# Optimization experiments

Hardware: AMD Instinct MI355X
Metric: run time of the kernel (lower is better)

Reference implementation:

```python
import jax, jax.numpy as jnp
import numpy as np

B, S, D, H = 4, 1024, 1024, 16
HD = D // H
LN_EPS = 1e-5


def setup_inputs() -> dict:
    key = jax.random.key(0)
    ks = jax.random.split(key, 16)
    def lin(k, fan_in, fan_out):
        bound = 1.0 / np.sqrt(fan_in)
        kw, kb = jax.random.split(k)
        W = jax.random.uniform(kw, (fan_in, fan_out), jnp.float32, -bound, bound)
        b = jax.random.uniform(kb, (fan_out,), jnp.float32, -bound, bound)
        return W, b
    W_attn, b_attn = lin(ks[0], D, 3 * D)   # self-attn fused QKV
    W_Q, b_Q = lin(ks[1], D, D)             # cross-attn Q
    W_KV, b_KV = lin(ks[2], D, 2 * D)       # cross-attn KV
    W1, b1 = lin(ks[3], D, 4 * D)           # FFN up
    W2, b2 = lin(ks[4], 4 * D, D)           # FFN down
    return {
        'en': jax.random.normal(ks[5], (B, S, D), jnp.float32),
        'fr': jax.random.normal(ks[6], (B, S, D), jnp.float32),
        'W_attn': W_attn, 'b_attn': b_attn,
        'W_Q': W_Q, 'b_Q': b_Q, 'W_KV': W_KV, 'b_KV': b_KV,
        'ln_g': jnp.ones((D,), jnp.float32), 'ln_b': jnp.zeros((D,), jnp.float32),
        'W1': W1, 'b1': b1, 'W2': W2, 'b2': b2,
        'l_en': jax.random.randint(ks[7], (B,), 1, S + 1, jnp.int32),
        'l_fr': jax.random.randint(ks[8], (B,), 1, S + 1, jnp.int32),
    }


def _masked_softmax(s):
    # softmax with rows that may be entirely -inf -> all-zero row (torch softmax + nan_to_num)
    m = jnp.max(s, axis=-1, keepdims=True)
    m = jnp.where(jnp.isfinite(m), m, 0.0)
    e = jnp.exp(s - m)  # exp(-inf) = 0
    z = jnp.sum(e, axis=-1, keepdims=True)
    return jnp.where(z > 0, e / jnp.where(z > 0, z, 1.0), 0.0)


def _layer_norm(x, g, b):
    mu = jnp.mean(x, axis=-1, keepdims=True)
    var = jnp.mean((x - mu) ** 2, axis=-1, keepdims=True)
    return (x - mu) * jax.lax.rsqrt(var + LN_EPS) * g + b


def _attend(q, k, v, mask):
    # q,k,v: [B,H,S,hd]; mask: [B,1|H broadcastable,S,S] of {0,1}
    scores = jnp.einsum('bhqd,bhkd->bhqk', q, k) / (D ** 0.5)  # NOTE: scaled by sqrt(D), as in source
    scores = jnp.where(mask == 0, -jnp.inf, scores)
    p = _masked_softmax(scores)
    out = jnp.einsum('bhqk,bhkd->bhqd', p, v)
    return out.transpose(0, 2, 1, 3).reshape(q.shape[0], q.shape[2], D)


def _valid(l):
    return (jnp.arange(S)[None, :] < l[:, None]).astype(jnp.float32)  # [B,S]


def reference(en, fr, W_attn, b_attn, W_Q, b_Q, W_KV, b_KV, ln_g, ln_b, W1, b1, W2, b2, l_en, l_fr):
    # dropout layers are identity in eval/reference mode
    v_en, v_fr = _valid(l_en), _valid(l_fr)

    # --- masked causal self-attention on fr ---
    rc = fr
    qkv = (fr @ W_attn + b_attn).reshape(B, S, 3, H, HD).transpose(2, 0, 3, 1, 4)
    q, k, v = qkv[0], qkv[1], qkv[2]
    pad = (v_fr[:, :, None] * v_fr[:, None, :])[:, None]            # [B,1,S,S]
    causal = jnp.tril(jnp.ones((S, S), jnp.float32))[None, None]    # [1,1,S,S]
    x = _attend(q, k, v, pad * causal)
    fr2 = _layer_norm(x + rc, ln_g, ln_b)

    # --- encoder-decoder cross attention ---
    rc = fr2
    q = (fr2 @ W_Q + b_Q).reshape(B, S, H, HD).transpose(0, 2, 1, 3)
    kv = (en @ W_KV + b_KV).reshape(B, S, 2, H, HD).transpose(2, 0, 3, 1, 4)
    k, v = kv[0], kv[1]
    cross = (v_fr[:, :, None] * v_en[:, None, :])[:, None]          # [B,1,S,S]
    x = _attend(q, k, v, cross)
    fr3 = _layer_norm(x + rc, ln_g, ln_b)

    # --- FFN (Linear->ReLU->Linear) then extra ReLU, residual, LN ---
    rc = fr3
    h = jax.nn.relu(fr3 @ W1 + b1) @ W2 + b2
    h = jax.nn.relu(h)
    fr4 = _layer_norm(h + rc, ln_g, ln_b)
    return fr4
```

## Files before the change

### kernel.cpp

```cpp
#include <hip/hip_runtime.h>
#include <hip/hip_bf16.h>
#include <cstdint>
#include <cstddef>

#define S_LEN  1024
#define DMODEL 1024
#define NHEAD  16
#define HDIM   64
#define BATCH  4
#define MROWS  (BATCH * S_LEN)

typedef __bf16 bf16;
typedef __attribute__((ext_vector_type(8))) __bf16 bf16x8;
typedef __attribute__((ext_vector_type(4))) __bf16 bf16x4;
typedef __attribute__((ext_vector_type(4))) float f32x4;
typedef __attribute__((ext_vector_type(4))) unsigned int u32x4;

__device__ __forceinline__ void async_load16(const void* g, void* l) {
    __builtin_amdgcn_global_load_lds(
        (const __attribute__((address_space(1))) unsigned int*)g,
        (__attribute__((address_space(3))) unsigned int*)l,
        16, 0, 0);
}

__global__ __launch_bounds__(256)
void prep_all(const float* __restrict__ fr, bf16* __restrict__ fr_bf,
              const float* __restrict__ en, bf16* __restrict__ en_bf,
              const float* __restrict__ Wa, bf16* __restrict__ Ta,
              const float* __restrict__ Wkv, bf16* __restrict__ Tkv) {
    __shared__ float t[32][33];
    int id = blockIdx.x;
    if (id < 8192) {
        const int n4 = MROWS * DMODEL / 4;
        int i = id * 256 + threadIdx.x;
        const float* in = fr; bf16* out = fr_bf;
        if (i >= n4) { i -= n4; in = en; out = en_bf; }
        f32x4 v = ((const f32x4*)in)[i];
        bf16x4 o;
#pragma unroll
        for (int e = 0; e < 4; ++e) o[e] = (bf16)v[e];
        ((bf16x4*)out)[i] = o;
        return;
    }
    id -= 8192;
    const float* W; bf16* Wt; int K, N, nx, base;
    if (id < 3072) { W = Wa;  Wt = Ta;  K = 1024; N = 3072; nx = 96; base = 0; }
    else           { W = Wkv; Wt = Tkv; K = 1024; N = 2048; nx = 64; base = 3072; }
    int loc = id - base;
    int n0 = (loc % nx) * 32, k0 = (loc / nx) * 32;
    int tx = threadIdx.x & 31, ty = threadIdx.x >> 5;
#pragma unroll
    for (int j = 0; j < 4; ++j)
        t[ty + j * 8][tx] = W[(size_t)(k0 + ty + j * 8) * N + n0 + tx];
    __syncthreads();
#pragma unroll
    for (int j = 0; j < 4; ++j)
        Wt[(size_t)(n0 + ty + j * 8) * K + k0 + tx] = (bf16)t[tx][ty + j * 8];
}

__device__ __forceinline__ void gemm_acc(const bf16* __restrict__ A,
                                         const bf16* __restrict__ Bt,
                                         int Klen, int lda, int ldb,
                                         bf16* Alds, bf16* Blds,
                                         f32x4 acc[4][4]) {
    const int tid = threadIdx.x;
    const int wave = tid >> 6, lane = tid & 63;
    const int wr = wave >> 1, wc = wave & 1;
    const int lr = lane & 15, lg = lane >> 4, lk = lg * 8;
    const int srow = lane >> 2, scol = (lane & 3) * 8;

    const bf16* Aw = A + (size_t)(wave * 32 + srow) * lda + scol;
    const bf16* Bw = Bt + (size_t)(wave * 32 + srow) * ldb + scol;
    const int ldsw = (wave * 32) * 32;

    async_load16(Aw, Alds + ldsw);
    async_load16(Aw + (size_t)16 * lda, Alds + ldsw + 16 * 32);
    async_load16(Bw, Blds + ldsw);
    async_load16(Bw + (size_t)16 * ldb, Blds + ldsw + 16 * 32);
    __syncthreads();

    const int nt = Klen >> 5;
    for (int t = 0; t < nt; ++t) {
        const int cur = t & 1;
        if (t + 1 < nt) {
            const size_t k0 = (size_t)(t + 1) << 5;
            bf16* Ad = Alds + (cur ^ 1) * (128 * 32) + ldsw;
            bf16* Bd = Blds + (cur ^ 1) * (128 * 32) + ldsw;
            async_load16(Aw + k0, Ad);
            async_load16(Aw + (size_t)16 * lda + k0, Ad + 16 * 32);
            async_load16(Bw + k0, Bd);
            async_load16(Bw + (size_t)16 * ldb + k0, Bd + 16 * 32);
        }
        const bf16* Ab = Alds + cur * (128 * 32);
        const bf16* Bb = Blds + cur * (128 * 32);
        bf16x8 af[4], bfv[4];
#pragma unroll
        for (int i = 0; i < 4; ++i) {
            af[i]  = *(const bf16x8*)&Ab[(wr * 64 + i * 16 + lr) * 32 + lk];
            bfv[i] = *(const bf16x8*)&Bb[(wc * 64 + i * 16 + lr) * 32 + lk];
        }
#pragma unroll
        for (int mi = 0; mi < 4; ++mi)
#pragma unroll
            for (int ni = 0; ni < 4; ++ni)
                acc[mi][ni] = __builtin_amdgcn_mfma_f32_16x16x32_bf16(
                    af[mi], bfv[ni], acc[mi][ni], 0, 0, 0);
        __syncthreads();
    }
}

__device__ __forceinline__ void gemm_acc64(const bf16* __restrict__ A,
                                           const bf16* __restrict__ Bt,
                                           int Klen, int lda, int ldb,
                                           bf16* Alds, bf16* Blds,
                                           f32x4 acc[4][4]) {
    const int tid = threadIdx.x;
    const int wave = tid >> 6, lane = tid & 63;
    const int wr = wave >> 1, wc = wave & 1;
    const int lr = lane & 15, lg = lane >> 4;
    const int srow = lane >> 3;
    const int sch = (lane & 7) ^ srow;

    const bf16* Aw = A + (size_t)(wave * 32 + srow) * lda + sch * 8;
    const bf16* Bw = Bt + (size_t)(wave * 32 + srow) * ldb + sch * 8;

    const int nt = Klen >> 6;
#define STAGE64(buf, k0)                                                       \
    {                                                                          \
        bf16* Ad = Alds + (buf) * (128 * 64) + (wave * 32) * 64;               \
        bf16* Bd = Blds + (buf) * (128 * 64) + (wave * 32) * 64;               \
        _Pragma("unroll")                                                      \
        for (int j = 0; j < 4; ++j) {                                          \
            async_load16(Aw + (size_t)(j * 8) * lda + (k0), Ad + (j * 8) * 64);\
            async_load16(Bw + (size_t)(j * 8) * ldb + (k0), Bd + (j * 8) * 64);\
        }                                                                      \
    }

    STAGE64(0, 0);
    __syncthreads();

    for (int t = 0; t < nt; ++t) {
        const int cur = t & 1;
        if (t + 1 < nt) STAGE64(cur ^ 1, (size_t)(t + 1) << 6);
        const char* Ab = (const char*)(Alds + cur * (128 * 64));
        const char* Bb = (const char*)(Blds + cur * (128 * 64));
#pragma unroll
        for (int ks = 0; ks < 2; ++ks) {
            bf16x8 af[4], bfv[4];
#pragma unroll
            for (int i = 0; i < 4; ++i) {
                int ra = wr * 64 + i * 16 + lr;
                int rb = wc * 64 + i * 16 + lr;
                af[i] = *(const bf16x8*)(Ab + (size_t)ra * 128 +
                          ((ks * 64 + lg * 16) ^ ((ra & 7) << 4)));
                bfv[i] = *(const bf16x8*)(Bb + (size_t)rb * 128 +
                          ((ks * 64 + lg * 16) ^ ((rb & 7) << 4)));
            }
#pragma unroll
            for (int mi = 0; mi < 4; ++mi)
#pragma unroll
                for (int ni = 0; ni < 4; ++ni)
                    acc[mi][ni] = __builtin_amdgcn_mfma_f32_16x16x32_bf16(
                        af[mi], bfv[ni], acc[mi][ni], 0, 0, 0);
        }
        __syncthreads();
    }
#undef STAGE64
}

template<bool RELU>
__device__ __forceinline__ void epi_bf16(bf16* __restrict__ C, const float* __restrict__ bias,
                                         int N, int m0, int n0, f32x4 acc[4][4]) {
    const int tid = threadIdx.x;
    const int wave = tid >> 6, lane = tid & 63;
    const int wr = wave >> 1, wc = wave & 1;
    const int lr = lane & 15, lg = lane >> 4;
#pragma unroll
    for (int ni = 0; ni < 4; ++ni) {
        int n = n0 + wc * 64 + ni * 16 + lr;
        float bn = bias[n];
#pragma unroll
        for (int mi = 0; mi < 4; ++mi)
#pragma unroll
            for (int r = 0; r < 4; ++r) {
                int m = m0 + wr * 64 + mi * 16 + lg * 4 + r;
                float v = acc[mi][ni][r] + bn;
                if (RELU) v = v > 0.f ? v : 0.f;
                C[(size_t)m * N + n] = (bf16)v;
            }
    }
}

__device__ __forceinline__ bool tile_dead(const int* Lm, int m0) {
    if (!Lm) return false;
    int cap = (Lm[m0 >> 10] + 63) & ~63;
    return (m0 & 1023) >= cap;
}

template<bool RELU>
__global__ __launch_bounds__(256, 2)
void gemm_one(const bf16* __restrict__ A, const bf16* __restrict__ Bt,
              const float* __restrict__ bias, bf16* __restrict__ C,
              int N, int K, const int* __restrict__ Lm) {
    __shared__ alignas(16) bf16 Alds[2][128 * 32];
    __shared__ alignas(16) bf16 Blds[2][128 * 32];
    const int nwg = gridDim.x;
    const int flat = blockIdx.x;
    const int swz = (flat & 7) * (nwg >> 3) + (flat >> 3);
    const int m0 = (swz & 31) * 128, n0 = (swz >> 5) * 128;
    if (tile_dead(Lm, m0)) return;
    f32x4 acc[4][4] = {};
    gemm_acc(A + (size_t)m0 * K, Bt + (size_t)n0 * K, K, K, K,
             &Alds[0][0], &Blds[0][0], acc);
    epi_bf16<RELU>(C, bias, N, m0, n0, acc);
}

template<bool RELU>
__global__ __launch_bounds__(256, 2)
void gemm_one64(const bf16* __restrict__ A, const bf16* __restrict__ Bt,
                const float* __restrict__ bias, bf16* __restrict__ C,
                int N, int K, const int* __restrict__ Lm) {
    __shared__ alignas(16) bf16 Alds[2][128 * 64];
    __shared__ alignas(16) bf16 Blds[2][128 * 64];
    const int nwg = gridDim.x;
    const int flat = blockIdx.x;
    const int swz = (flat & 7) * (nwg >> 3) + (flat >> 3);
    const int m0 = (swz & 31) * 128, n0 = (swz >> 5) * 128;
    if (tile_dead(Lm, m0)) return;
    f32x4 acc[4][4] = {};
    gemm_acc64(A + (size_t)m0 * K, Bt + (size_t)n0 * K, K, K, K,
               &Alds[0][0], &Blds[0][0], acc);
    epi_bf16<RELU>(C, bias, N, m0, n0, acc);
}

struct GemmArgs {
    const bf16* A; const bf16* Bt; const float* bias; bf16* C;
    int N; int K; const int* Lm;
};
__global__ __launch_bounds__(256, 2)
void gemm_dual(GemmArgs g0, int nwg0, GemmArgs g1, int nwgG,
               const float* __restrict__ Wq, bf16* __restrict__ Tq,
               const float* __restrict__ W1, bf16* __restrict__ T1,
               const float* __restrict__ W2, bf16* __restrict__ T2) {
    __shared__ alignas(16) bf16 Alds[2][128 * 32];
    __shared__ alignas(16) bf16 Blds[2][128 * 32];
    const int flat = blockIdx.x;
    if (flat >= nwgG) {
        int id = flat - nwgG;
        const float* W; bf16* Wt; int K, N, nx, base;
        if (id < 1024)      { W = Wq; Wt = Tq; K = 1024; N = 1024; nx = 32;  base = 0; }
        else if (id < 5120) { W = W1; Wt = T1; K = 1024; N = 4096; nx = 128; base = 1024; }
        else                { W = W2; Wt = T2; K = 4096; N = 1024; nx = 32;  base = 5120; }
        int loc = id - base;
        int n0 = (loc % nx) * 32, k0 = (loc / nx) * 32;
        float (*t)[33] = (float(*)[33])&Alds[0][0];
        int tx = threadIdx.x & 31, ty = threadIdx.x >> 5;
#pragma unroll
        for (int j = 0; j < 4; ++j)
            t[ty + j * 8][tx] = W[(size_t)(k0 + ty + j * 8) * N + n0 + tx];
        __syncthreads();
#pragma unroll
        for (int j = 0; j < 4; ++j)
            Wt[(size_t)(n0 + ty + j * 8) * K + k0 + tx] = (bf16)t[tx][ty + j * 8];
        return;
    }
    const int swz = (flat & 7) * (nwgG >> 3) + (flat >> 3);
    const bool first = swz < nwg0;
    const GemmArgs g = first ? g0 : g1;
    const int f = first ? swz : swz - nwg0;
    const int m0 = (f & 31) * 128, n0 = (f >> 5) * 128;
    if (tile_dead(g.Lm, m0)) return;
    f32x4 acc[4][4] = {};
    gemm_acc(g.A + (size_t)m0 * g.K, g.Bt + (size_t)n0 * g.K, g.K, g.K, g.K,
             &Alds[0][0], &Blds[0][0], acc);
    epi_bf16<false>(g.C, g.bias, g.N, m0, n0, acc);
}

__global__ __launch_bounds__(256, 2)
void gemm_splitk2(const bf16* __restrict__ A, const bf16* __restrict__ Bt,
                  float* __restrict__ P0, float* __restrict__ P1,
                  int N, int K, int nwg_half) {
    __shared__ alignas(16) bf16 Alds[2][128 * 64];
    __shared__ alignas(16) bf16 Blds[2][128 * 64];
    const int nwg = gridDim.x;
    const int flat = blockIdx.x;
    const int swz = (flat & 7) * (nwg >> 3) + (flat >> 3);
    const int kz = swz >= nwg_half ? 1 : 0;
    const int f = swz - kz * nwg_half;
    const int m0 = (f & 31) * 128, n0 = (f >> 5) * 128;
    const int Kh = K >> 1;
    const size_t koff = (size_t)kz * Kh;
    f32x4 acc[4][4] = {};
    gemm_acc64(A + (size_t)m0 * K + koff, Bt + (size_t)n0 * K + koff, Kh, K, K,
               &Alds[0][0], &Blds[0][0], acc);
    float* P = kz ? P1 : P0;
    const int tid = threadIdx.x;
    const int wave = tid >> 6, lane = tid & 63;
    const int wr = wave >> 1, wc = wave & 1;
    const int lr = lane & 15, lg = lane >> 4;
#pragma unroll
    for (int ni = 0; ni < 4; ++ni) {
        int n = n0 + wc * 64 + ni * 16 + lr;
#pragma unroll
        for (int mi = 0; mi < 4; ++mi)
#pragma unroll
            for (int r = 0; r < 4; ++r) {
                int m = m0 + wr * 64 + mi * 16 + lg * 4 + r;
                P[(size_t)m * N + n] = acc[mi][ni][r];
            }
    }
}

template<bool CAUSAL>
__global__ __launch_bounds__(256, 4)
void attn_flash(const bf16* __restrict__ Qp, int qs,
                const bf16* __restrict__ Kp, int ks,
                const bf16* __restrict__ Vp, int vs,
                const int* __restrict__ Lq, const int* __restrict__ Lk,
                bf16* __restrict__ Op) {
    __shared__ alignas(16) bf16 Klds[64 * 64];
    __shared__ alignas(16) bf16 Vt[64 * 64];
    __shared__ alignas(16) bf16 Plds[4][16 * 64];

    const int tid = threadIdx.x;
    const int wave = tid >> 6, lane = tid & 63;
    const int h = blockIdx.y, b = blockIdx.z;
    const int qt = (blockIdx.x + (b << 2)) & 15;
    const int q0 = qt * 64;
    const int lq = Lq[b], lk = Lk[b];
    const int lr = lane & 15, lg = lane >> 4;

    if (q0 >= lq) {
#pragma unroll
        for (int dt = 0; dt < 4; ++dt)
#pragma unroll
            for (int r = 0; r < 4; ++r) {
                int q = q0 + wave * 16 + lg * 4 + r;
                Op[(size_t)(b * S_LEN + q) * DMODEL + h * HDIM + dt * 16 + lr] = (bf16)0.f;
            }
        return;
    }

    char* KldsB = (char*)Klds;
    char* VtB = (char*)Vt;
    char* PldsB = (char*)&Plds[wave][0];

    bf16x8 aq[2];
    {
        const bf16* qrow = Qp + (size_t)(b * S_LEN + q0 + wave * 16 + lr) * qs + h * HDIM;
        aq[0] = *(const bf16x8*)(qrow + 0 + lg * 8);
        aq[1] = *(const bf16x8*)(qrow + 32 + lg * 8);
    }

    f32x4 o[4] = {};
    float m_run[4], l_run[4];
#pragma unroll
    for (int r = 0; r < 4; ++r) { m_run[r] = -INFINITY; l_run[r] = 0.f; }

    int kv_end = CAUSAL ? (q0 + 64) : S_LEN;
    int lk_cap = (lk + 63) & ~63;
    if (kv_end > lk_cap) kv_end = lk_cap;

    const int vk = lane;
    const int vd0 = wave * 16;

    for (int kk0 = 0; kk0 < kv_end; kk0 += 64) {
#pragma unroll
        for (int c = 0; c < 2; ++c) {
            int rloc = c * 8 + (lane >> 3);
            int row = wave * 16 + rloc;
            int chunk = (lane & 7) ^ (rloc & 7);
            async_load16(Kp + (size_t)(b * S_LEN + kk0 + row) * ks + h * HDIM + chunk * 8,
                         KldsB + (size_t)(wave * 16 + c * 8) * 128);
        }
        {
            const bf16* vsrc = Vp + (size_t)(b * S_LEN + kk0 + vk) * vs + h * HDIM + vd0;
            bf16x8 v0 = *(const bf16x8*)vsrc;
            bf16x8 v1 = *(const bf16x8*)(vsrc + 8);
#pragma unroll
            for (int e = 0; e < 8; ++e) {
                int d0 = vd0 + e, d1 = vd0 + 8 + e;
                *(bf16*)(VtB + (((size_t)d0 * 128 + vk * 2) ^ ((d0 & 7) << 4))) = v0[e];
                *(bf16*)(VtB + (((size_t)d1 * 128 + vk * 2) ^ ((d1 & 7) << 4))) = v1[e];
            }
        }
        __syncthreads();

        f32x4 sa[4];
#pragma unroll
        for (int kt = 0; kt < 4; ++kt) {
            int row = kt * 16 + lr;
            f32x4 z = {};
#pragma unroll
            for (int ds_ = 0; ds_ < 2; ++ds_) {
                bf16x8 bk = *(const bf16x8*)(KldsB +
                    (((size_t)row * 128 + ds_ * 64 + lg * 16) ^ ((row & 7) << 4)));
                z = __builtin_amdgcn_mfma_f32_16x16x32_bf16(aq[ds_], bk, z, 0, 0, 0);
            }
            sa[kt] = z;
        }

        float p[4][4];
#pragma unroll
        for (int r = 0; r < 4; ++r) {
            int q = q0 + wave * 16 + lg * 4 + r;
            float best = -INFINITY;
#pragma unroll
            for (int kt = 0; kt < 4; ++kt) {
                int kk = kk0 + kt * 16 + lr;
                float s = sa[kt][r] * 0.03125f;
                bool ok = (q < lq) && (kk < lk) && (!CAUSAL || kk <= q);
                s = ok ? s : -INFINITY;
                p[kt][r] = s;
                best = fmaxf(best, s);
            }
#pragma unroll
            for (int msk = 1; msk < 16; msk <<= 1)
                best = fmaxf(best, __shfl_xor(best, msk));
            float mn = fmaxf(m_run[r], best);
            float alpha = (m_run[r] == -INFINITY) ? 0.0f : __expf(m_run[r] - mn);
            float rs = 0.f;
#pragma unroll
            for (int kt = 0; kt < 4; ++kt) {
                float s = p[kt][r];
                float e = (s == -INFINITY) ? 0.f : __expf(s - mn);
                p[kt][r] = e;
                rs += e;
            }
#pragma unroll
            for (int msk = 1; msk < 16; msk <<= 1)
                rs += __shfl_xor(rs, msk);
            l_run[r] = l_run[r] * alpha + rs;
            m_run[r] = mn;
#pragma unroll
            for (int dt = 0; dt < 4; ++dt) o[dt][r] *= alpha;
        }

#pragma unroll
        for (int kt = 0; kt < 4; ++kt)
#pragma unroll
            for (int r = 0; r < 4; ++r) {
                int ql = lg * 4 + r, kkl = kt * 16 + lr;
                *(bf16*)(PldsB + (((size_t)ql * 128 + kkl * 2) ^ ((ql & 7) << 4))) =
                    (bf16)p[kt][r];
            }
        bf16x8 pa[2];
#pragma unroll
        for (int ksl = 0; ksl < 2; ++ksl)
            pa[ksl] = *(const bf16x8*)(PldsB +
                (((size_t)lr * 128 + ksl * 64 + lg * 16) ^ ((lr & 7) << 4)));

#pragma unroll
        for (int dt = 0; dt < 4; ++dt) {
            int row = dt * 16 + lr;
#pragma unroll
            for (int ksl = 0; ksl < 2; ++ksl) {
                bf16x8 bv = *(const bf16x8*)(VtB +
                    (((size_t)row * 128 + ksl * 64 + lg * 16) ^ ((row & 7) << 4)));
                o[dt] = __builtin_amdgcn_mfma_f32_16x16x32_bf16(pa[ksl], bv, o[dt], 0, 0, 0);
            }
        }
        __syncthreads();
    }

#pragma unroll
    for (int dt = 0; dt < 4; ++dt) {
#pragma unroll
        for (int r = 0; r < 4; ++r) {
            int q = q0 + wave * 16 + lg * 4 + r;
            float denom = l_run[r];
            float val = denom > 0.f ? o[dt][r] / denom : 0.f;
            Op[(size_t)(b * S_LEN + q) * DMODEL + h * HDIM + dt * 16 + lr] = (bf16)val;
        }
    }
}

template<bool RC_F32>
__global__ __launch_bounds__(256)
void ln_kernel(const bf16* __restrict__ x, const void* __restrict__ rc,
               const float* __restrict__ g, const float* __restrict__ beta,
               bf16* __restrict__ yb) {
    const int row = blockIdx.x;
    const int tid = threadIdx.x;
    const int wave = tid >> 6, lane = tid & 63;
    const bf16* xr = x + (size_t)row * DMODEL;

    float v[4];
    {
        bf16x4 xv = *(const bf16x4*)(xr + tid * 4);
        if (RC_F32) {
            f32x4 rv = *(const f32x4*)((const float*)rc + (size_t)row * DMODEL + tid * 4);
#pragma unroll
            for (int i = 0; i < 4; ++i) v[i] = (float)xv[i] + rv[i];
        } else {
            bf16x4 rv = *(const bf16x4*)((const bf16*)rc + (size_t)row * DMODEL + tid * 4);
#pragma unroll
            for (int i = 0; i < 4; ++i) v[i] = (float)xv[i] + (float)rv[i];
        }
    }
    float s = v[0] + v[1] + v[2] + v[3];
    float s2 = v[0] * v[0] + v[1] * v[1] + v[2] * v[2] + v[3] * v[3];
#pragma unroll
    for (int msk = 1; msk < 64; msk <<= 1) {
        s += __shfl_xor(s, msk);
        s2 += __shfl_xor(s2, msk);
    }
    __shared__ float red[8];
    if (lane == 0) { red[wave] = s; red[4 + wave] = s2; }
    __syncthreads();
    float ts = red[0] + red[1] + red[2] + red[3];
    float ts2 = red[4] + red[5] + red[6] + red[7];
    float mean = ts * (1.f / DMODEL);
    float var = ts2 * (1.f / DMODEL) - mean * mean;
    float inv = rsqrtf(var + 1e-5f);
    bf16x4 o;
#pragma unroll
    for (int i = 0; i < 4; ++i) {
        int c = tid * 4 + i;
        o[i] = (bf16)((v[i] - mean) * inv * g[c] + beta[c]);
    }
    *(bf16x4*)(yb + (size_t)row * DMODEL + tid * 4) = o;
}

__global__ __launch_bounds__(256)
void ln_splitk(const float* __restrict__ P0, const float* __restrict__ P1,
               const float* __restrict__ bias, const bf16* __restrict__ rc,
               const float* __restrict__ g, const float* __restrict__ beta,
               float* __restrict__ yf) {
    const int row = blockIdx.x;
    const int tid = threadIdx.x;
    const int wave = tid >> 6, lane = tid & 63;
    const size_t off = (size_t)row * DMODEL + tid * 4;

    f32x4 a = *(const f32x4*)(P0 + off);
    f32x4 bb = *(const f32x4*)(P1 + off);
    f32x4 bi = *(const f32x4*)(bias + tid * 4);
    bf16x4 rv = *(const bf16x4*)(rc + off);
    float v[4];
#pragma unroll
    for (int i = 0; i < 4; ++i) {
        float h = a[i] + bb[i] + bi[i];
        h = h > 0.f ? h : 0.f;
        v[i] = h + (float)rv[i];
    }
    float s = v[0] + v[1] + v[2] + v[3];
    float s2 = v[0] * v[0] + v[1] * v[1] + v[2] * v[2] + v[3] * v[3];
#pragma unroll
    for (int msk = 1; msk < 64; msk <<= 1) {
        s += __shfl_xor(s, msk);
        s2 += __shfl_xor(s2, msk);
    }
    __shared__ float red[8];
    if (lane == 0) { red[wave] = s; red[4 + wave] = s2; }
    __syncthreads();
    float ts = red[0] + red[1] + red[2] + red[3];
    float ts2 = red[4] + red[5] + red[6] + red[7];
    float mean = ts * (1.f / DMODEL);
    float var = ts2 * (1.f / DMODEL) - mean * mean;
    float inv = rsqrtf(var + 1e-5f);
#pragma unroll
    for (int i = 0; i < 4; ++i) {
        int c = tid * 4 + i;
        yf[(size_t)row * DMODEL + c] = (v[i] - mean) * inv * g[c] + beta[c];
    }
}

extern "C" void kernel_launch(void* const* d_in, const int* in_sizes, int n_in,
                              void* d_out, int out_size, void* d_ws, size_t ws_size,
                              hipStream_t stream) {
    const float* en     = (const float*)d_in[0];
    const float* fr     = (const float*)d_in[1];
    const float* W_attn = (const float*)d_in[2];
    const float* b_attn = (const float*)d_in[3];
    const float* W_Q    = (const float*)d_in[4];
    const float* b_Q    = (const float*)d_in[5];
    const float* W_KV   = (const float*)d_in[6];
    const float* b_KV   = (const float*)d_in[7];
    const float* ln_g   = (const float*)d_in[8];
    const float* ln_b   = (const float*)d_in[9];
    const float* W1     = (const float*)d_in[10];
    const float* b1     = (const float*)d_in[11];
    const float* W2     = (const float*)d_in[12];
    const float* b2     = (const float*)d_in[13];
    const int* l_en     = (const int*)d_in[14];
    const int* l_fr     = (const int*)d_in[15];
    float* out = (float*)d_out;

    char* ws = (char*)d_ws;
    const size_t MB = (size_t)1 << 20;
    bf16* Wt_attn = (bf16*)(ws + 0);
    bf16* Wt_Q    = (bf16*)(ws + 6 * MB);
    bf16* Wt_KV   = (bf16*)(ws + 8 * MB);
    bf16* Wt_1    = (bf16*)(ws + 12 * MB);
    bf16* Wt_2    = (bf16*)(ws + 20 * MB);
    bf16* fr_bf   = (bf16*)(ws + 28 * MB);
    bf16* en_bf   = (bf16*)(ws + 36 * MB);
    bf16* bigA    = (bf16*)(ws + 44 * MB);
    bf16* xbuf    = (bf16*)(ws + 76 * MB);
    bf16* y1      = (bf16*)(ws + 116 * MB);
    bf16* y2      = (bf16*)(ws + 84 * MB);
    float* P0 = (float*)(ws + 0);
    float* P1 = (float*)(ws + 28 * MB);
    bf16* kvc = (bf16*)(ws + 100 * MB);

    dim3 blk(256);

    prep_all<<<dim3(13312), blk, 0, stream>>>(fr, fr_bf, en, en_bf,
                                              W_attn, Wt_attn, W_KV, Wt_KV);

    bf16* qkv = bigA;
    GemmArgs gq{fr_bf, Wt_attn, b_attn, qkv, 3072, 1024, l_fr};
    GemmArgs gk{en_bf, Wt_KV, b_KV, kvc, 2048, 1024, l_en};
    gemm_dual<<<dim3(1280 + 9216), blk, 0, stream>>>(gq, 768, gk, 1280,
                                                     W_Q, Wt_Q, W1, Wt_1, W2, Wt_2);

    attn_flash<true><<<dim3(16, NHEAD, BATCH), blk, 0, stream>>>(
        qkv, 3072, qkv + 1024, 3072, qkv + 2048, 3072, l_fr, l_fr, xbuf);
    ln_kernel<true><<<dim3(4096), blk, 0, stream>>>(xbuf, fr, ln_g, ln_b, y1);

    bf16* qc = bigA;
    gemm_one64<false><<<dim3(256), blk, 0, stream>>>(y1, Wt_Q, b_Q, qc, 1024, 1024, l_fr);
    attn_flash<false><<<dim3(16, NHEAD, BATCH), blk, 0, stream>>>(
        qc, 1024, kvc, 2048, kvc + 1024, 2048, l_fr, l_en, xbuf);
    ln_kernel<false><<<dim3(4096), blk, 0, stream>>>(xbuf, y1, ln_g, ln_b, y2);

    bf16* h = bigA;
    gemm_one<true><<<dim3(1024), blk, 0, stream>>>(y2, Wt_1, b1, h, 4096, 1024, nullptr);
    gemm_splitk2<<<dim3(512), blk, 0, stream>>>(h, Wt_2, P0, P1, 1024, 4096, 256);
    ln_splitk<<<dim3(4096), blk, 0, stream>>>(P0, P1, b2, y2, ln_g, ln_b, out);
}
```

Measured before the change: 267.1 us.

## Overlap cross-attn KV GEMM with causal self-attention and lazily rescale softmax

Moves the en→KV projection GEMM out of the QKV/weight-transpose launch and into the same grid as the causal self-attention kernel. The two independent workloads then share the GPU and attention's tail can be filled by GEMM tiles. The attention body also skips the running-max rescale unless the new max exceeds the old one by more than 8, and wraps the MFMA sections in s_setprio. The fused kernel uses 32KB of shared memory with a 4-blocks-per-SM launch bound, so occupancy may change, and the lazy rescale relies on fp32 headroom for exponents up to e^8.

Result: slower. 280.3 us (+5.0%).

```diff
diff --git a/kernel.cpp b/kernel.cpp
--- a/kernel.cpp
+++ b/kernel.cpp
@@ -15,6 +15,8 @@
 typedef __attribute__((ext_vector_type(4))) __bf16 bf16x4;
 typedef __attribute__((ext_vector_type(4))) float f32x4;
 typedef __attribute__((ext_vector_type(4))) unsigned int u32x4;
+
+#define PRIO(x) __builtin_amdgcn_s_setprio(x)
 
 __device__ __forceinline__ void async_load16(const void* g, void* l) {
     __builtin_amdgcn_global_load_lds(
@@ -195,6 +197,251 @@
     if (!Lm) return false;
     int cap = (Lm[m0 >> 10] + 63) & ~63;
     return (m0 & 1023) >= cap;
+}
+
+template<bool CAUSAL>
+__device__ __forceinline__ void attn_body(char* smemB, int qt, int h, int b,
+                                          const bf16* __restrict__ Qp, int qs,
+                                          const bf16* __restrict__ Kp, int ks,
+                                          const bf16* __restrict__ Vp, int vs,
+                                          int lq, int lk, bf16* __restrict__ Op) {
+    const int tid = threadIdx.x;
+    const int wave = tid >> 6, lane = tid & 63;
+    const int q0 = qt * 64;
+    const int lr = lane & 15, lg = lane >> 4;
+
+    if (q0 >= lq) {
+#pragma unroll
+        for (int dt = 0; dt < 4; ++dt)
+#pragma unroll
+            for (int r = 0; r < 4; ++r) {
+                int q = q0 + wave * 16 + lg * 4 + r;
+                Op[(size_t)(b * S_LEN + q) * DMODEL + h * HDIM + dt * 16 + lr] = (bf16)0.f;
+            }
+        return;
+    }
+
+    char* KldsB = smemB;
+    char* VtB = smemB + 8192;
+    char* PldsB = smemB + 16384 + wave * 2048;
+
+    bf16x8 aq[2];
+    {
+        const bf16* qrow = Qp + (size_t)(b * S_LEN + q0 + wave * 16 + lr) * qs + h * HDIM;
+        aq[0] = *(const bf16x8*)(qrow + 0 + lg * 8);
+        aq[1] = *(const bf16x8*)(qrow + 32 + lg * 8);
+    }
+
+    f32x4 o[4] = {};
+    float m_run[4], l_run[4];
+#pragma unroll
+    for (int r = 0; r < 4; ++r) { m_run[r] = -INFINITY; l_run[r] = 0.f; }
+
+    int kv_end = CAUSAL ? (q0 + 64) : S_LEN;
+    int lk_cap = (lk + 63) & ~63;
+    if (kv_end > lk_cap) kv_end = lk_cap;
+
+    const int vk = lane;
+    const int vd0 = wave * 16;
+
+    for (int kk0 = 0; kk0 < kv_end; kk0 += 64) {
+#pragma unroll
+        for (int c = 0; c < 2; ++c) {
+            int rloc = c * 8 + (lane >> 3);
+            int row = wave * 16 + rloc;
+            int chunk = (lane & 7) ^ (rloc & 7);
+            async_load16(Kp + (size_t)(b * S_LEN + kk0 + row) * ks + h * HDIM + chunk * 8,
+                         KldsB + (size_t)(wave * 16 + c * 8) * 128);
+        }
+        {
+            const bf16* vsrc = Vp + (size_t)(b * S_LEN + kk0 + vk) * vs + h * HDIM + vd0;
+            bf16x8 v0 = *(const bf16x8*)vsrc;
+            bf16x8 v1 = *(const bf16x8*)(vsrc + 8);
+#pragma unroll
+            for (int e = 0; e < 8; ++e) {
+                int d0 = vd0 + e, d1 = vd0 + 8 + e;
+                *(bf16*)(VtB + (((size_t)d0 * 128 + vk * 2) ^ ((d0 & 7) << 4))) = v0[e];
+                *(bf16*)(VtB + (((size_t)d1 * 128 + vk * 2) ^ ((d1 & 7) << 4))) = v1[e];
+            }
+        }
+        __syncthreads();
+
+        f32x4 sa[4];
+        PRIO(1);
+#pragma unroll
+        for (int kt = 0; kt < 4; ++kt) {
+            int row = kt * 16 + lr;
+            f32x4 z = {};
+#pragma unroll
+            for (int ds_ = 0; ds_ < 2; ++ds_) {
+                bf16x8 bk = *(const bf16x8*)(KldsB +
+                    (((size_t)row * 128 + ds_ * 64 + lg * 16) ^ ((row & 7) << 4)));
+                z = __builtin_amdgcn_mfma_f32_16x16x32_bf16(aq[ds_], bk, z, 0, 0, 0);
+            }
+            sa[kt] = z;
+        }
+        PRIO(0);
+
+        float p[4][4];
+#pragma unroll
+        for (int r = 0; r < 4; ++r) {
+            int q = q0 + wave * 16 + lg * 4 + r;
+            float best = -INFINITY;
+#pragma unroll
+            for (int kt = 0; kt < 4; ++kt) {
+                int kk = kk0 + kt * 16 + lr;
+                float s = sa[kt][r] * 0.03125f;
+                bool ok = (q < lq) && (kk < lk) && (!CAUSAL || kk <= q);
+                s = ok ? s : -INFINITY;
+                p[kt][r] = s;
+                best = fmaxf(best, s);
+            }
+#pragma unroll
+            for (int msk = 1; msk < 16; msk <<= 1)
+                best = fmaxf(best, __shfl_xor(best, msk));
+            float mo = m_run[r];
+            if (!(best <= mo + 8.f)) {
+                float mn = fmaxf(mo, best);
+                float alpha = (mo == -INFINITY) ? 0.f : __expf(mo - mn);
+                l_run[r] *= alpha;
+#pragma unroll
+                for (int dt = 0; dt < 4; ++dt) o[dt][r] *= alpha;
+                m_run[r] = mn;
+            }
+            float mc = m_run[r];
+            float rs = 0.f;
+#pragma unroll
+            for (int kt = 0; kt < 4; ++kt) {
+                float s = p[kt][r];
+                float e = (s == -INFINITY) ? 0.f : __expf(s - mc);
+                p[kt][r] = e;
+                rs += e;
+            }
+#pragma unroll
+            for (int msk = 1; msk < 16; msk <<= 1)
+                rs += __shfl_xor(rs, msk);
+            l_run[r] += rs;
+        }
+
+#pragma unroll
+        for (int kt = 0; kt < 4; ++kt)
+#pragma unroll
+            for (int r = 0; r < 4; ++r) {
+                int ql = lg * 4 + r, kkl = kt * 16 + lr;
+                *(bf16*)(PldsB + (((size_t)ql * 128 + kkl * 2) ^ ((ql & 7) << 4))) =
+                    (bf16)p[kt][r];
+            }
+        bf16x8 pa[2];
+#pragma unroll
+        for (int ksl = 0; ksl < 2; ++ksl)
+            pa[ksl] = *(const bf16x8*)(PldsB +
+                (((size_t)lr * 128 + ksl * 64 + lg * 16) ^ ((lr & 7) << 4)));
+
+        PRIO(1);
+#pragma unroll
+        for (int dt = 0; dt < 4; ++dt) {
+            int row = dt * 16 + lr;
+#pragma unroll
+            for (int ksl = 0; ksl < 2; ++ksl) {
+                bf16x8 bv = *(const bf16x8*)(VtB +
+                    (((size_t)row * 128 + ksl * 64 + lg * 16) ^ ((row & 7) << 4)));
+                o[dt] = __builtin_amdgcn_mfma_f32_16x16x32_bf16(pa[ksl], bv, o[dt], 0, 0, 0);
+            }
+        }
+        PRIO(0);
+        __syncthreads();
+    }
+
+#pragma unroll
+    for (int dt = 0; dt < 4; ++dt) {
+#pragma unroll
+        for (int r = 0; r < 4; ++r) {
+            int q = q0 + wave * 16 + lg * 4 + r;
+            float denom = l_run[r];
+            float val = denom > 0.f ? o[dt][r] / denom : 0.f;
+            Op[(size_t)(b * S_LEN + q) * DMODEL + h * HDIM + dt * 16 + lr] = (bf16)val;
+        }
+    }
+}
+
+__global__ __launch_bounds__(256, 4)
+void attn1_fused(const bf16* __restrict__ Qp, int qs,
+                 const bf16* __restrict__ Kp, int ks,
+                 const bf16* __restrict__ Vp, int vs,
+                 const int* __restrict__ Lq, bf16* __restrict__ Op,
+                 const bf16* __restrict__ gA, const bf16* __restrict__ gBt,
+                 const float* __restrict__ gbias, bf16* __restrict__ gC,
+                 int gN, int gK, const int* __restrict__ gLm, int nwgG) {
+    __shared__ alignas(16) char smem[32768];
+    const int flat = blockIdx.x;
+    if (flat < nwgG) {
+        const int swz = (flat & 7) * (nwgG >> 3) + (flat >> 3);
+        const int m0 = (swz & 31) * 128, n0 = (swz >> 5) * 128;
+        if (tile_dead(gLm, m0)) return;
+        f32x4 acc[4][4] = {};
+        gemm_acc(gA + (size_t)m0 * gK, gBt + (size_t)n0 * gK, gK, gK, gK,
+                 (bf16*)smem, (bf16*)(smem + 16384), acc);
+        epi_bf16<false>(gC, gbias, gN, m0, n0, acc);
+        return;
+    }
+    const int f2 = flat - nwgG;
+    const int b = f2 >> 8, h = (f2 >> 4) & 15;
+    const int qt = ((f2 & 15) + (b << 2)) & 15;
+    const int lq = Lq[b];
+    attn_body<true>(smem, qt, h, b, Qp, qs, Kp, ks, Vp, vs, lq, lq, Op);
+}
+
+template<bool CAUSAL>
+__global__ __launch_bounds__(256, 4)
+void attn_flash(const bf16* __restrict__ Qp, int qs,
+                const bf16* __restrict__ Kp, int ks,
+                const bf16* __restrict__ Vp, int vs,
+                const int* __restrict__ Lq, const int* __restrict__ Lk,
+                bf16* __restrict__ Op) {
+    __shared__ alignas(16) char smem[24576];
+    const int h = blockIdx.y, b = blockIdx.z;
+    const int qt = (blockIdx.x + (b << 2)) & 15;
+    attn_body<CAUSAL>(smem, qt, h, b, Qp, qs, Kp, ks, Vp, vs, Lq[b], Lk[b], Op);
+}
+
+struct GemmArgs {
+    const bf16* A; const bf16* Bt; const float* bias; bf16* C;
+    int N; int K; const int* Lm;
+};
+__global__ __launch_bounds__(256, 2)
+void gemm_qkv_wt(GemmArgs g, int nwgG,
+                 const float* __restrict__ Wq, bf16* __restrict__ Tq,
+                 const float* __restrict__ W1, bf16* __restrict__ T1,
+                 const float* __restrict__ W2, bf16* __restrict__ T2) {
+    __shared__ alignas(16) bf16 Alds[2][128 * 32];
+    __shared__ alignas(16) bf16 Blds[2][128 * 32];
+    const int flat = blockIdx.x;
+    if (flat >= nwgG) {
+        int id = flat - nwgG;
+        const float* W; bf16* Wt; int K, N, nx, base;
+        if (id < 1024)      { W = Wq; Wt = Tq; K = 1024; N = 1024; nx = 32;  base = 0; }
+        else if (id < 5120) { W = W1; Wt = T1; K = 1024; N = 4096; nx = 128; base = 1024; }
+        else                { W = W2; Wt = T2; K = 4096; N = 1024; nx = 32;  base = 5120; }
+        int loc = id - base;
+        int n0 = (loc % nx) * 32, k0 = (loc / nx) * 32;
+        float (*t)[33] = (float(*)[33])&Alds[0][0];
+        int tx = threadIdx.x & 31, ty = threadIdx.x >> 5;
+#pragma unroll
+        for (int j = 0; j < 4; ++j)
+            t[ty + j * 8][tx] = W[(size_t)(k0 + ty + j * 8) * N + n0 + tx];
+        __syncthreads();
+#pragma unroll
+        for (int j = 0; j < 4; ++j)
+            Wt[(size_t)(n0 + ty + j * 8) * K + k0 + tx] = (bf16)t[tx][ty + j * 8];
+        return;
+    }
+    const int swz = (flat & 7) * (nwgG >> 3) + (flat >> 3);
+    const int m0 = (swz & 31) * 128, n0 = (swz >> 5) * 128;
+    if (tile_dead(g.Lm, m0)) return;
+    f32x4 acc[4][4] = {};
+    gemm_acc(g.A + (size_t)m0 * g.K, g.Bt + (size_t)n0 * g.K, g.K, g.K, g.K,
+             &Alds[0][0], &Blds[0][0], acc);
+    epi_bf16<false>(g.C, g.bias, g.N, m0, n0, acc);
 }
 
 template<bool RELU>
@@ -231,49 +478,6 @@
     gemm_acc64(A + (size_t)m0 * K, Bt + (size_t)n0 * K, K, K, K,
                &Alds[0][0], &Blds[0][0], acc);
     epi_bf16<RELU>(C, bias, N, m0, n0, acc);
-}
-
-struct GemmArgs {
-    const bf16* A; const bf16* Bt; const float* bias; bf16* C;
-    int N; int K; const int* Lm;
-};
-__global__ __launch_bounds__(256, 2)
-void gemm_dual(GemmArgs g0, int nwg0, GemmArgs g1, int nwgG,
-               const float* __restrict__ Wq, bf16* __restrict__ Tq,
-               const float* __restrict__ W1, bf16* __restrict__ T1,
-               const float* __restrict__ W2, bf16* __restrict__ T2) {
-    __shared__ alignas(16) bf16 Alds[2][128 * 32];
-    __shared__ alignas(16) bf16 Blds[2][128 * 32];
-    const int flat = blockIdx.x;
-    if (flat >= nwgG) {
-        int id = flat - nwgG;
-        const float* W; bf16* Wt; int K, N, nx, base;
-        if (id < 1024)      { W = Wq; Wt = Tq; K = 1024; N = 1024; nx = 32;  base = 0; }
-        else if (id < 5120) { W = W1; Wt = T1; K = 1024; N = 4096; nx = 128; base = 1024; }
-        else                { W = W2; Wt = T2; K = 4096; N = 1024; nx = 32;  base = 5120; }
-        int loc = id - base;
-        int n0 = (loc % nx) * 32, k0 = (loc / nx) * 32;
-        float (*t)[33] = (float(*)[33])&Alds[0][0];
-        int tx = threadIdx.x & 31, ty = threadIdx.x >> 5;
-#pragma unroll
-        for (int j = 0; j < 4; ++j)
-            t[ty + j * 8][tx] = W[(size_t)(k0 + ty + j * 8) * N + n0 + tx];
-        __syncthreads();
-#pragma unroll
-        for (int j = 0; j < 4; ++j)
-            Wt[(size_t)(n0 + ty + j * 8) * K + k0 + tx] = (bf16)t[tx][ty + j * 8];
-        return;
-    }
-    const int swz = (flat & 7) * (nwgG >> 3) + (flat >> 3);
-    const bool first = swz < nwg0;
-    const GemmArgs g = first ? g0 : g1;
-    const int f = first ? swz : swz - nwg0;
-    const int m0 = (f & 31) * 128, n0 = (f >> 5) * 128;
-    if (tile_dead(g.Lm, m0)) return;
-    f32x4 acc[4][4] = {};
-    gemm_acc(g.A + (size_t)m0 * g.K, g.Bt + (size_t)n0 * g.K, g.K, g.K, g.K,
-             &Alds[0][0], &Blds[0][0], acc);
-    epi_bf16<false>(g.C, g.bias, g.N, m0, n0, acc);
 }
 
 __global__ __launch_bounds__(256, 2)
@@ -311,170 +515,6 @@
     }
 }
 
-template<bool CAUSAL>
-__global__ __launch_bounds__(256, 4)
-void attn_flash(const bf16* __restrict__ Qp, int qs,
-                const bf16* __restrict__ Kp, int ks,
-                const bf16* __restrict__ Vp, int vs,
-                const int* __restrict__ Lq, const int* __restrict__ Lk,
-                bf16* __restrict__ Op) {
-    __shared__ alignas(16) bf16 Klds[64 * 64];
-    __shared__ alignas(16) bf16 Vt[64 * 64];
-    __shared__ alignas(16) bf16 Plds[4][16 * 64];
-
-    const int tid = threadIdx.x;
-    const int wave = tid >> 6, lane = tid & 63;
-    const int h = blockIdx.y, b = blockIdx.z;
-    const int qt = (blockIdx.x + (b << 2)) & 15;
-    const int q0 = qt * 64;
-    const int lq = Lq[b], lk = Lk[b];
-    const int lr = lane & 15, lg = lane >> 4;
-
-    if (q0 >= lq) {
-#pragma unroll
-        for (int dt = 0; dt < 4; ++dt)
-#pragma unroll
-            for (int r = 0; r < 4; ++r) {
-                int q = q0 + wave * 16 + lg * 4 + r;
-                Op[(size_t)(b * S_LEN + q) * DMODEL + h * HDIM + dt * 16 + lr] = (bf16)0.f;
-            }
-        return;
-    }
-
-    char* KldsB = (char*)Klds;
-    char* VtB = (char*)Vt;
-    char* PldsB = (char*)&Plds[wave][0];
-
-    bf16x8 aq[2];
-    {
-        const bf16* qrow = Qp + (size_t)(b * S_LEN + q0 + wave * 16 + lr) * qs + h * HDIM;
-        aq[0] = *(const bf16x8*)(qrow + 0 + lg * 8);
-        aq[1] = *(const bf16x8*)(qrow + 32 + lg * 8);
-    }
-
-    f32x4 o[4] = {};
-    float m_run[4], l_run[4];
-#pragma unroll
-    for (int r = 0; r < 4; ++r) { m_run[r] = -INFINITY; l_run[r] = 0.f; }
-
-    int kv_end = CAUSAL ? (q0 + 64) : S_LEN;
-    int lk_cap = (lk + 63) & ~63;
-    if (kv_end > lk_cap) kv_end = lk_cap;
-
-    const int vk = lane;
-    const int vd0 = wave * 16;
-
-    for (int kk0 = 0; kk0 < kv_end; kk0 += 64) {
-#pragma unroll
-        for (int c = 0; c < 2; ++c) {
-            int rloc = c * 8 + (lane >> 3);
-            int row = wave * 16 + rloc;
-            int chunk = (lane & 7) ^ (rloc & 7);
-            async_load16(Kp + (size_t)(b * S_LEN + kk0 + row) * ks + h * HDIM + chunk * 8,
-                         KldsB + (size_t)(wave * 16 + c * 8) * 128);
-        }
-        {
-            const bf16* vsrc = Vp + (size_t)(b * S_LEN + kk0 + vk) * vs + h * HDIM + vd0;
-            bf16x8 v0 = *(const bf16x8*)vsrc;
-            bf16x8 v1 = *(const bf16x8*)(vsrc + 8);
-#pragma unroll
-            for (int e = 0; e < 8; ++e) {
-                int d0 = vd0 + e, d1 = vd0 + 8 + e;
-                *(bf16*)(VtB + (((size_t)d0 * 128 + vk * 2) ^ ((d0 & 7) << 4))) = v0[e];
-                *(bf16*)(VtB + (((size_t)d1 * 128 + vk * 2) ^ ((d1 & 7) << 4))) = v1[e];
-            }
-        }
-        __syncthreads();
-
-        f32x4 sa[4];
-#pragma unroll
-        for (int kt = 0; kt < 4; ++kt) {
-            int row = kt * 16 + lr;
-            f32x4 z = {};
-#pragma unroll
-            for (int ds_ = 0; ds_ < 2; ++ds_) {
-                bf16x8 bk = *(const bf16x8*)(KldsB +
-                    (((size_t)row * 128 + ds_ * 64 + lg * 16) ^ ((row & 7) << 4)));
-                z = __builtin_amdgcn_mfma_f32_16x16x32_bf16(aq[ds_], bk, z, 0, 0, 0);
-            }
-            sa[kt] = z;
-        }
-
-        float p[4][4];
-#pragma unroll
-        for (int r = 0; r < 4; ++r) {
-            int q = q0 + wave * 16 + lg * 4 + r;
-            float best = -INFINITY;
-#pragma unroll
-            for (int kt = 0; kt < 4; ++kt) {
-                int kk = kk0 + kt * 16 + lr;
-                float s = sa[kt][r] * 0.03125f;
-                bool ok = (q < lq) && (kk < lk) && (!CAUSAL || kk <= q);
-                s = ok ? s : -INFINITY;
-                p[kt][r] = s;
-                best = fmaxf(best, s);
-            }
-#pragma unroll
-            for (int msk = 1; msk < 16; msk <<= 1)
-                best = fmaxf(best, __shfl_xor(best, msk));
-            float mn = fmaxf(m_run[r], best);
-            float alpha = (m_run[r] == -INFINITY) ? 0.0f : __expf(m_run[r] - mn);
-            float rs = 0.f;
-#pragma unroll
-            for (int kt = 0; kt < 4; ++kt) {
-                float s = p[kt][r];
-                float e = (s == -INFINITY) ? 0.f : __expf(s - mn);
-                p[kt][r] = e;
-                rs += e;
-            }
-#pragma unroll
-            for (int msk = 1; msk < 16; msk <<= 1)
-                rs += __shfl_xor(rs, msk);
-            l_run[r] = l_run[r] * alpha + rs;
-            m_run[r] = mn;
-#pragma unroll
-            for (int dt = 0; dt < 4; ++dt) o[dt][r] *= alpha;
-        }
-
-#pragma unroll
-        for (int kt = 0; kt < 4; ++kt)
-#pragma unroll
-            for (int r = 0; r < 4; ++r) {
-                int ql = lg * 4 + r, kkl = kt * 16 + lr;
-                *(bf16*)(PldsB + (((size_t)ql * 128 + kkl * 2) ^ ((ql & 7) << 4))) =
-                    (bf16)p[kt][r];
-            }
-        bf16x8 pa[2];
-#pragma unroll
-        for (int ksl = 0; ksl < 2; ++ksl)
-            pa[ksl] = *(const bf16x8*)(PldsB +
-                (((size_t)lr * 128 + ksl * 64 + lg * 16) ^ ((lr & 7) << 4)));
-
-#pragma unroll
-        for (int dt = 0; dt < 4; ++dt) {
-            int row = dt * 16 + lr;
-#pragma unroll
-            for (int ksl = 0; ksl < 2; ++ksl) {
-                bf16x8 bv = *(const bf16x8*)(VtB +
-                    (((size_t)row * 128 + ksl * 64 + lg * 16) ^ ((row & 7) << 4)));
-                o[dt] = __builtin_amdgcn_mfma_f32_16x16x32_bf16(pa[ksl], bv, o[dt], 0, 0, 0);
-            }
-        }
-        __syncthreads();
-    }
-
-#pragma unroll
-    for (int dt = 0; dt < 4; ++dt) {
-#pragma unroll
-        for (int r = 0; r < 4; ++r) {
-            int q = q0 + wave * 16 + lg * 4 + r;
-            float denom = l_run[r];
-            float val = denom > 0.f ? o[dt][r] / denom : 0.f;
-            Op[(size_t)(b * S_LEN + q) * DMODEL + h * HDIM + dt * 16 + lr] = (bf16)val;
-        }
-    }
-}
-
 template<bool RC_F32>
 __global__ __launch_bounds__(256)
 void ln_kernel(const bf16* __restrict__ x, const void* __restrict__ rc,
@@ -610,12 +650,12 @@
 
     bf16* qkv = bigA;
     GemmArgs gq{fr_bf, Wt_attn, b_attn, qkv, 3072, 1024, l_fr};
-    GemmArgs gk{en_bf, Wt_KV, b_KV, kvc, 2048, 1024, l_en};
-    gemm_dual<<<dim3(1280 + 9216), blk, 0, stream>>>(gq, 768, gk, 1280,
-                                                     W_Q, Wt_Q, W1, Wt_1, W2, Wt_2);
-
-    attn_flash<true><<<dim3(16, NHEAD, BATCH), blk, 0, stream>>>(
-        qkv, 3072, qkv + 1024, 3072, qkv + 2048, 3072, l_fr, l_fr, xbuf);
+    gemm_qkv_wt<<<dim3(768 + 9216), blk, 0, stream>>>(gq, 768,
+                                                      W_Q, Wt_Q, W1, Wt_1, W2, Wt_2);
+
+    attn1_fused<<<dim3(512 + 1024), blk, 0, stream>>>(
+        qkv, 3072, qkv + 1024, 3072, qkv + 2048, 3072, l_fr, xbuf,
+        en_bf, Wt_KV, b_KV, kvc, 2048, 1024, l_en, 512);
     ln_kernel<true><<<dim3(4096), blk, 0, stream>>>(xbuf, fr, ln_g, ln_b, y1);
 
     bf16* qc = bigA;
```

## Process two 64-row query sub-tiles per attention block to reuse K/V tiles

Applied to the files above, without the earlier changes.

Each flash-attention block now handles 128 query rows as two 64-row sub-tiles that share every K and V tile loaded into LDS. This halves the grid and the K/V global loads and transposes per query row. In the causal case the first sub-tile skips the final KV tile. In exchange each thread holds twice the accumulators and softmax state, so register pressure rises and launch bounds drop to 2 blocks per CU. There are also fewer blocks overall, which can hurt load balance given the causal and length-based work skew.

After: 310.5 us. +16.3%, slower.

```diff
diff --git a/kernel.cpp b/kernel.cpp
--- a/kernel.cpp
+++ b/kernel.cpp
@@ -312,59 +312,63 @@
 }
 
 template<bool CAUSAL>
-__global__ __launch_bounds__(256, 4)
+__global__ __launch_bounds__(256, 2)
 void attn_flash(const bf16* __restrict__ Qp, int qs,
                 const bf16* __restrict__ Kp, int ks,
                 const bf16* __restrict__ Vp, int vs,
                 const int* __restrict__ Lq, const int* __restrict__ Lk,
                 bf16* __restrict__ Op) {
-    __shared__ alignas(16) bf16 Klds[64 * 64];
-    __shared__ alignas(16) bf16 Vt[64 * 64];
-    __shared__ alignas(16) bf16 Plds[4][16 * 64];
+    __shared__ alignas(16) char smem[32768];
 
     const int tid = threadIdx.x;
     const int wave = tid >> 6, lane = tid & 63;
     const int h = blockIdx.y, b = blockIdx.z;
-    const int qt = (blockIdx.x + (b << 2)) & 15;
-    const int q0 = qt * 64;
+    const int qt = (blockIdx.x + (b << 1)) & 7;
+    const int q0 = qt * 128;
     const int lq = Lq[b], lk = Lk[b];
     const int lr = lane & 15, lg = lane >> 4;
 
     if (q0 >= lq) {
 #pragma unroll
-        for (int dt = 0; dt < 4; ++dt)
-#pragma unroll
-            for (int r = 0; r < 4; ++r) {
-                int q = q0 + wave * 16 + lg * 4 + r;
-                Op[(size_t)(b * S_LEN + q) * DMODEL + h * HDIM + dt * 16 + lr] = (bf16)0.f;
-            }
+        for (int s = 0; s < 2; ++s)
+#pragma unroll
+            for (int dt = 0; dt < 4; ++dt)
+#pragma unroll
+                for (int r = 0; r < 4; ++r) {
+                    int q = q0 + s * 64 + wave * 16 + lg * 4 + r;
+                    Op[(size_t)(b * S_LEN + q) * DMODEL + h * HDIM + dt * 16 + lr] = (bf16)0.f;
+                }
         return;
     }
 
-    char* KldsB = (char*)Klds;
-    char* VtB = (char*)Vt;
-    char* PldsB = (char*)&Plds[wave][0];
-
-    bf16x8 aq[2];
-    {
-        const bf16* qrow = Qp + (size_t)(b * S_LEN + q0 + wave * 16 + lr) * qs + h * HDIM;
-        aq[0] = *(const bf16x8*)(qrow + 0 + lg * 8);
-        aq[1] = *(const bf16x8*)(qrow + 32 + lg * 8);
-    }
-
-    f32x4 o[4] = {};
-    float m_run[4], l_run[4];
-#pragma unroll
-    for (int r = 0; r < 4; ++r) { m_run[r] = -INFINITY; l_run[r] = 0.f; }
-
-    int kv_end = CAUSAL ? (q0 + 64) : S_LEN;
-    int lk_cap = (lk + 63) & ~63;
-    if (kv_end > lk_cap) kv_end = lk_cap;
+    char* KldsB = smem;
+    char* VtB = smem + 8192;
+
+    bf16x8 aq[2][2];
+#pragma unroll
+    for (int s = 0; s < 2; ++s) {
+        const bf16* qrow = Qp + (size_t)(b * S_LEN + q0 + s * 64 + wave * 16 + lr) * qs + h * HDIM;
+        aq[s][0] = *(const bf16x8*)(qrow + 0 + lg * 8);
+        aq[s][1] = *(const bf16x8*)(qrow + 32 + lg * 8);
+    }
+
+    f32x4 o[2][4] = {};
+    float m_run[2][4], l_run[2][4];
+#pragma unroll
+    for (int s = 0; s < 2; ++s)
+#pragma unroll
+        for (int r = 0; r < 4; ++r) { m_run[s][r] = -INFINITY; l_run[s][r] = 0.f; }
+
+    const int lk_cap = (lk + 63) & ~63;
+    int end0 = CAUSAL ? (q0 + 64) : S_LEN;
+    int end1 = CAUSAL ? (q0 + 128) : S_LEN;
+    if (end0 > lk_cap) end0 = lk_cap;
+    if (end1 > lk_cap) end1 = lk_cap;
 
     const int vk = lane;
     const int vd0 = wave * 16;
 
-    for (int kk0 = 0; kk0 < kv_end; kk0 += 64) {
+    for (int kk0 = 0; kk0 < end1; kk0 += 64) {
 #pragma unroll
         for (int c = 0; c < 2; ++c) {
             int rloc = c * 8 + (lane >> 3);
@@ -386,93 +390,101 @@
         }
         __syncthreads();
 
-        f32x4 sa[4];
-#pragma unroll
-        for (int kt = 0; kt < 4; ++kt) {
-            int row = kt * 16 + lr;
-            f32x4 z = {};
-#pragma unroll
-            for (int ds_ = 0; ds_ < 2; ++ds_) {
-                bf16x8 bk = *(const bf16x8*)(KldsB +
-                    (((size_t)row * 128 + ds_ * 64 + lg * 16) ^ ((row & 7) << 4)));
-                z = __builtin_amdgcn_mfma_f32_16x16x32_bf16(aq[ds_], bk, z, 0, 0, 0);
-            }
-            sa[kt] = z;
-        }
-
-        float p[4][4];
-#pragma unroll
-        for (int r = 0; r < 4; ++r) {
-            int q = q0 + wave * 16 + lg * 4 + r;
-            float best = -INFINITY;
+#pragma unroll
+        for (int s = 0; s < 2; ++s) {
+            if (s == 0 && kk0 >= end0) continue;
+            char* PldsB = smem + 16384 + s * 8192 + wave * 2048;
+            const int qb = q0 + s * 64;
+
+            f32x4 sa[4];
 #pragma unroll
             for (int kt = 0; kt < 4; ++kt) {
-                int kk = kk0 + kt * 16 + lr;
-                float s = sa[kt][r] * 0.03125f;
-                bool ok = (q < lq) && (kk < lk) && (!CAUSAL || kk <= q);
-                s = ok ? s : -INFINITY;
-                p[kt][r] = s;
-                best = fmaxf(best, s);
-            }
-#pragma unroll
-            for (int msk = 1; msk < 16; msk <<= 1)
-                best = fmaxf(best, __shfl_xor(best, msk));
-            float mn = fmaxf(m_run[r], best);
-            float alpha = (m_run[r] == -INFINITY) ? 0.0f : __expf(m_run[r] - mn);
-            float rs = 0.f;
-#pragma unroll
-            for (int kt = 0; kt < 4; ++kt) {
-                float s = p[kt][r];
-                float e = (s == -INFINITY) ? 0.f : __expf(s - mn);
-                p[kt][r] = e;
-                rs += e;
-            }
-#pragma unroll
-            for (int msk = 1; msk < 16; msk <<= 1)
-                rs += __shfl_xor(rs, msk);
-            l_run[r] = l_run[r] * alpha + rs;
-            m_run[r] = mn;
-#pragma unroll
-            for (int dt = 0; dt < 4; ++dt) o[dt][r] *= alpha;
-        }
-
-#pragma unroll
-        for (int kt = 0; kt < 4; ++kt)
+                int row = kt * 16 + lr;
+                f32x4 z = {};
+#pragma unroll
+                for (int ds_ = 0; ds_ < 2; ++ds_) {
+                    bf16x8 bk = *(const bf16x8*)(KldsB +
+                        (((size_t)row * 128 + ds_ * 64 + lg * 16) ^ ((row & 7) << 4)));
+                    z = __builtin_amdgcn_mfma_f32_16x16x32_bf16(aq[s][ds_], bk, z, 0, 0, 0);
+                }
+                sa[kt] = z;
+            }
+
+            float p[4][4];
 #pragma unroll
             for (int r = 0; r < 4; ++r) {
-                int ql = lg * 4 + r, kkl = kt * 16 + lr;
-                *(bf16*)(PldsB + (((size_t)ql * 128 + kkl * 2) ^ ((ql & 7) << 4))) =
-                    (bf16)p[kt][r];
-            }
-        bf16x8 pa[2];
-#pragma unroll
-        for (int ksl = 0; ksl < 2; ++ksl)
-            pa[ksl] = *(const bf16x8*)(PldsB +
-                (((size_t)lr * 128 + ksl * 64 + lg * 16) ^ ((lr & 7) << 4)));
-
-#pragma unroll
-        for (int dt = 0; dt < 4; ++dt) {
-            int row = dt * 16 + lr;
-#pragma unroll
-            for (int ksl = 0; ksl < 2; ++ksl) {
-                bf16x8 bv = *(const bf16x8*)(VtB +
-                    (((size_t)row * 128 + ksl * 64 + lg * 16) ^ ((row & 7) << 4)));
-                o[dt] = __builtin_amdgcn_mfma_f32_16x16x32_bf16(pa[ksl], bv, o[dt], 0, 0, 0);
+                int q = qb + wave * 16 + lg * 4 + r;
+                float best = -INFINITY;
+#pragma unroll
+                for (int kt = 0; kt < 4; ++kt) {
+                    int kk = kk0 + kt * 16 + lr;
+                    float sv = sa[kt][r] * 0.03125f;
+                    bool ok = (q < lq) && (kk < lk) && (!CAUSAL || kk <= q);
+                    sv = ok ? sv : -INFINITY;
+                    p[kt][r] = sv;
+                    best = fmaxf(best, sv);
+                }
+#pragma unroll
+                for (int msk = 1; msk < 16; msk <<= 1)
+                    best = fmaxf(best, __shfl_xor(best, msk));
+                float mn = fmaxf(m_run[s][r], best);
+                float alpha = (m_run[s][r] == -INFINITY) ? 0.0f : __expf(m_run[s][r] - mn);
+                float rs = 0.f;
+#pragma unroll
+                for (int kt = 0; kt < 4; ++kt) {
+                    float sv = p[kt][r];
+                    float e = (sv == -INFINITY) ? 0.f : __expf(sv - mn);
+                    p[kt][r] = e;
+                    rs += e;
+                }
+#pragma unroll
+                for (int msk = 1; msk < 16; msk <<= 1)
+                    rs += __shfl_xor(rs, msk);
+                l_run[s][r] = l_run[s][r] * alpha + rs;
+                m_run[s][r] = mn;
+#pragma unroll
+                for (int dt = 0; dt < 4; ++dt) o[s][dt][r] *= alpha;
+            }
+
+#pragma unroll
+            for (int kt = 0; kt < 4; ++kt)
+#pragma unroll
+                for (int r = 0; r < 4; ++r) {
+                    int ql = lg * 4 + r, kkl = kt * 16 + lr;
+                    *(bf16*)(PldsB + (((size_t)ql * 128 + kkl * 2) ^ ((ql & 7) << 4))) =
+                        (bf16)p[kt][r];
+                }
+            bf16x8 pa[2];
+#pragma unroll
+            for (int ksl = 0; ksl < 2; ++ksl)
+                pa[ksl] = *(const bf16x8*)(PldsB +
+                    (((size_t)lr * 128 + ksl * 64 + lg * 16) ^ ((lr & 7) << 4)));
+
+#pragma unroll
+            for (int dt = 0; dt < 4; ++dt) {
+                int row = dt * 16 + lr;
+#pragma unroll
+                for (int ksl = 0; ksl < 2; ++ksl) {
+                    bf16x8 bv = *(const bf16x8*)(VtB +
+                        (((size_t)row * 128 + ksl * 64 + lg * 16) ^ ((row & 7) << 4)));
+                    o[s][dt] = __builtin_amdgcn_mfma_f32_16x16x32_bf16(pa[ksl], bv, o[s][dt], 0, 0, 0);
+                }
             }
         }
         __syncthreads();
     }
 
 #pragma unroll
-    for (int dt = 0; dt < 4; ++dt) {
-#pragma unroll
-        for (int r = 0; r < 4; ++r) {
-            int q = q0 + wave * 16 + lg * 4 + r;
-            float denom = l_run[r];
-            float val = denom > 0.f ? o[dt][r] / denom : 0.f;
-            Op[(size_t)(b * S_LEN + q) * DMODEL + h * HDIM + dt * 16 + lr] = (bf16)val;
-        }
-    }
+    for (int s = 0; s < 2; ++s)
+#pragma unroll
+        for (int dt = 0; dt < 4; ++dt)
+#pragma unroll
+            for (int r = 0; r < 4; ++r) {
+                int q = q0 + s * 64 + wave * 16 + lg * 4 + r;
+                float denom = l_run[s][r];
+                float val = denom > 0.f ? o[s][dt][r] / denom : 0.f;
+                Op[(size_t)(b * S_LEN + q) * DMODEL + h * HDIM + dt * 16 + lr] = (bf16)val;
+            }
 }
 
 template<bool RC_F32>
@@ -614,13 +626,13 @@
     gemm_dual<<<dim3(1280 + 9216), blk, 0, stream>>>(gq, 768, gk, 1280,
                                                      W_Q, Wt_Q, W1, Wt_1, W2, Wt_2);
 
-    attn_flash<true><<<dim3(16, NHEAD, BATCH), blk, 0, stream>>>(
+    attn_flash<true><<<dim3(8, NHEAD, BATCH), blk, 0, stream>>>(
         qkv, 3072, qkv + 1024, 3072, qkv + 2048, 3072, l_fr, l_fr, xbuf);
     ln_kernel<true><<<dim3(4096), blk, 0, stream>>>(xbuf, fr, ln_g, ln_b, y1);
 
     bf16* qc = bigA;
     gemm_one64<false><<<dim3(256), blk, 0, stream>>>(y1, Wt_Q, b_Q, qc, 1024, 1024, l_fr);
-    attn_flash<false><<<dim3(16, NHEAD, BATCH), blk, 0, stream>>>(
+    attn_flash<false><<<dim3(8, NHEAD, BATCH), blk, 0, stream>>>(
         qc, 1024, kvc, 2048, kvc + 1024, 2048, l_fr, l_en, xbuf);
     ln_kernel<false><<<dim3(4096), blk, 0, stream>>>(xbuf, y1, ln_g, ln_b, y2);
 
```
